# Kernel tuning notes

Hardware: AMD Instinct MI355X
Metric: run time of the kernel (lower is better)

## Reference

```python
import jax, jax.numpy as jnp
import numpy as np

D_MODEL = 1024
N_HEADS = 16
HEAD_DIM = D_MODEL // N_HEADS
D_FF = 4 * D_MODEL
LN_EPS = 1e-5


def setup_inputs() -> dict:
    key = jax.random.key(0)
    ks = jax.random.split(key, 12)
    B, T = 16, 512
    s = lambda fan_in: 1.0 / np.sqrt(fan_in)
    inp = {
        'x': jax.random.normal(ks[0], (B, T, D_MODEL), jnp.float32),
        # torch Linear layout: [out_features, in_features]
        'w_qkv': jax.random.normal(ks[1], (3 * D_MODEL, D_MODEL), jnp.float32) * s(D_MODEL),
        'w_proj': jax.random.normal(ks[2], (D_MODEL, D_MODEL), jnp.float32) * s(D_MODEL),
        'w_ff1': jax.random.normal(ks[3], (D_FF, D_MODEL), jnp.float32) * s(D_MODEL),
        'b_ff1': jax.random.normal(ks[4], (D_FF,), jnp.float32) * 0.02,
        'w_ff2': jax.random.normal(ks[5], (D_MODEL, D_FF), jnp.float32) * s(D_FF),
        'b_ff2': jax.random.normal(ks[6], (D_MODEL,), jnp.float32) * 0.02,
        'ln1_g': jnp.ones((D_MODEL,), jnp.float32),
        'ln1_b': jnp.zeros((D_MODEL,), jnp.float32),
        'ln2_g': jnp.ones((D_MODEL,), jnp.float32),
        'ln2_b': jnp.zeros((D_MODEL,), jnp.float32),
    }
    return inp


def _layernorm(x, g, b):
    mu = jnp.mean(x, axis=-1, keepdims=True)
    var = jnp.var(x, axis=-1, keepdims=True)
    return (x - mu) * jax.lax.rsqrt(var + LN_EPS) * g + b


def _block(x, w_qkv, w_proj, w_ff1, b_ff1, w_ff2, b_ff2, ln1_g, ln1_b, ln2_g, ln2_b):
    B, T, _ = x.shape
    a = _layernorm(x, ln1_g, ln1_b)
    qkv = a @ w_qkv.T  # [B,T,3D]
    q, k, v = jnp.split(qkv, 3, axis=-1)
    # [B,H,T,hd]
    rs = lambda t: t.reshape(B, T, N_HEADS, HEAD_DIM).transpose(0, 2, 1, 3)
    q, k, v = rs(q), rs(k), rs(v)
    scale = HEAD_DIM ** -0.5
    att = jnp.einsum('bhqd,bhkd->bhqk', q, k) * scale
    causal = jnp.tril(jnp.ones((T, T), bool))
    att = jnp.where(causal, att, jnp.float32(-10000.0))
    att = jax.nn.softmax(att, axis=-1)
    out = jnp.einsum('bhqk,bhkd->bhqd', att, v)
    out = out.transpose(0, 2, 1, 3).reshape(B, T, D_MODEL)
    x = x + out @ w_proj.T
    f = _layernorm(x, ln2_g, ln2_b)
    f = jax.nn.gelu(f @ w_ff1.T + b_ff1, approximate=False) @ w_ff2.T + b_ff2
    return x + f


def reference(x, w_qkv, w_proj, w_ff1, b_ff1, w_ff2, b_ff2, ln1_g, ln1_b, ln2_g, ln2_b):
    return _block(x, w_qkv, w_proj, w_ff1, b_ff1, w_ff2, b_ff2, ln1_g, ln1_b, ln2_g, ln2_b)
```

## Files before the change

### kernel.cpp

```cpp
#include <hip/hip_runtime.h>
#include <stdint.h>

typedef __bf16 bf16x8_t __attribute__((ext_vector_type(8)));
typedef float f32x4_t __attribute__((ext_vector_type(4)));
typedef unsigned short ushort8_t __attribute__((ext_vector_type(8)));

#define DEV __device__ __forceinline__

DEV unsigned short f2bf(float f) {
  union { float f; uint32_t u; } v; v.f = f;
  uint32_t r = v.u + 0x7FFFu + ((v.u >> 16) & 1u);
  return (unsigned short)(r >> 16);
}

DEV void gl_lds16(const void* g, void* l) {
  __builtin_amdgcn_global_load_lds(
      (const __attribute__((address_space(1))) void*)g,
      (__attribute__((address_space(3))) void*)l, 16, 0, 0);
}

DEV float gelu_f(float x) {
  const float y = x * 0.7071067811865475f;
  const float ay = fabsf(y);
  const float t = __builtin_amdgcn_rcpf(1.0f + 0.3275911f * ay);
  float p = fmaf(t, 1.061405429f, -1.453152027f);
  p = fmaf(t, p, 1.421413741f);
  p = fmaf(t, p, -0.284496736f);
  p = fmaf(t, p, 0.254829592f);
  p *= t;
  const float e = __expf(-ay * ay);
  float erfv = 1.0f - p * e;
  erfv = copysignf(erfv, y);
  return 0.5f * x * (1.0f + erfv);
}

__global__ __launch_bounds__(256) void cvt_all(const float* __restrict__ w0, unsigned short* __restrict__ o0,
                                               const float* __restrict__ w1, unsigned short* __restrict__ o1,
                                               const float* __restrict__ w2, unsigned short* __restrict__ o2,
                                               const float* __restrict__ w3, unsigned short* __restrict__ o3) {
  int i = blockIdx.x * 256 + threadIdx.x;
  const float* in; unsigned short* outp;
  if (i < 786432) { in = w0; outp = o0; }
  else if (i < 1048576) { in = w1; outp = o1; i -= 786432; }
  else if (i < 2097152) { in = w2; outp = o2; i -= 1048576; }
  else { in = w3; outp = o3; i -= 2097152; }
  float4 v = ((const float4*)in)[i];
  ushort4 o;
  o.x = f2bf(v.x); o.y = f2bf(v.y); o.z = f2bf(v.z); o.w = f2bf(v.w);
  ((ushort4*)outp)[i] = o;
}

__global__ __launch_bounds__(256) void ln_kernel(const float* __restrict__ x,
                                                 const float* __restrict__ g,
                                                 const float* __restrict__ b,
                                                 unsigned short* __restrict__ outp) {
  const int row = blockIdx.x * 4 + (threadIdx.x >> 6);
  const int lane = threadIdx.x & 63;
  const float4* xr = (const float4*)(x + (size_t)row * 1024);
  float4 v[4];
  float s = 0.f, s2 = 0.f;
#pragma unroll
  for (int j = 0; j < 4; ++j) {
    v[j] = xr[j * 64 + lane];
    s += v[j].x + v[j].y + v[j].z + v[j].w;
    s2 += v[j].x * v[j].x + v[j].y * v[j].y + v[j].z * v[j].z + v[j].w * v[j].w;
  }
#pragma unroll
  for (int off = 1; off < 64; off <<= 1) {
    s += __shfl_xor(s, off, 64);
    s2 += __shfl_xor(s2, off, 64);
  }
  const float mu = s * (1.0f / 1024.0f);
  const float var = s2 * (1.0f / 1024.0f) - mu * mu;
  const float rstd = rsqrtf(var + 1e-5f);
  ushort4* orow = (ushort4*)(outp + (size_t)row * 1024);
  const float4* gp = (const float4*)g;
  const float4* bp = (const float4*)b;
#pragma unroll
  for (int j = 0; j < 4; ++j) {
    float4 gv = gp[j * 64 + lane], bv = bp[j * 64 + lane];
    ushort4 o;
    o.x = f2bf((v[j].x - mu) * rstd * gv.x + bv.x);
    o.y = f2bf((v[j].y - mu) * rstd * gv.y + bv.y);
    o.z = f2bf((v[j].z - mu) * rstd * gv.z + bv.z);
    o.w = f2bf((v[j].w - mu) * rstd * gv.w + bv.w);
    orow[j * 64 + lane] = o;
  }
}

template <int MODE>
__global__ __launch_bounds__(256) void gemm_bt(const unsigned short* __restrict__ A,
                                               const unsigned short* __restrict__ B,
                                               float* __restrict__ Cf,
                                               unsigned short* __restrict__ Cb,
                                               const float* __restrict__ bias,
                                               const float* __restrict__ res,
                                               int M, int N, int K) {
  __shared__ unsigned short sA[128 * 32];
  __shared__ unsigned short sB[128 * 32];
  const int tid = threadIdx.x;
  const int w = tid >> 6, lane = tid & 63;
  const int kg = lane >> 4, l16 = lane & 15;
  const int wm = (w & 1) * 64, wn = (w >> 1) * 64;
  const int rowBase = blockIdx.y * 128, colBase = blockIdx.x * 128;

  const int ar = tid >> 2;
  const int ac = (((tid & 3) ^ ((tid >> 3) & 3))) * 8;
  const unsigned short* gA = A + (size_t)(rowBase + ar) * K + ac;
  const unsigned short* gB = B + (size_t)(colBase + ar) * K + ac;
  unsigned short* lA = sA + tid * 8;
  unsigned short* lB = sB + tid * 8;

  f32x4_t acc[4][4];
#pragma unroll
  for (int mi = 0; mi < 4; ++mi)
#pragma unroll
    for (int ni = 0; ni < 4; ++ni) acc[mi][ni] = (f32x4_t)0.0f;

  const unsigned short* pA[4];
  const unsigned short* pB[4];
#pragma unroll
  for (int i = 0; i < 4; ++i) {
    const int rr = wm + i * 16 + l16;
    pA[i] = sA + (rr * 4 + (kg ^ ((l16 >> 1) & 3))) * 8;
    const int cr = wn + i * 16 + l16;
    pB[i] = sB + (cr * 4 + (kg ^ ((l16 >> 1) & 3))) * 8;
  }

  const int nk = K >> 5;
  for (int kt = 0; kt < nk; ++kt) {
    __syncthreads();
    gl_lds16(gA, lA);
    gl_lds16(gA + (size_t)64 * K, lA + 64 * 32);
    gl_lds16(gB, lB);
    gl_lds16(gB + (size_t)64 * K, lB + 64 * 32);
    gA += 32; gB += 32;
    __syncthreads();
    bf16x8_t a[4], b[4];
#pragma unroll
    for (int i = 0; i < 4; ++i) a[i] = *(const bf16x8_t*)pA[i];
#pragma unroll
    for (int i = 0; i < 4; ++i) b[i] = *(const bf16x8_t*)pB[i];
#pragma unroll
    for (int mi = 0; mi < 4; ++mi)
#pragma unroll
      for (int ni = 0; ni < 4; ++ni)
        acc[mi][ni] = __builtin_amdgcn_mfma_f32_16x16x32_bf16(a[mi], b[ni], acc[mi][ni], 0, 0, 0);
  }

#pragma unroll
  for (int mi = 0; mi < 4; ++mi) {
#pragma unroll
    for (int ni = 0; ni < 4; ++ni) {
      const int col = colBase + wn + ni * 16 + l16;
      float bv = 0.f;
      if (MODE == 2 || MODE == 3) bv = bias[col];
#pragma unroll
      for (int r = 0; r < 4; ++r) {
        const int row = rowBase + wm + mi * 16 + kg * 4 + r;
        const size_t idx = (size_t)row * N + col;
        float v = acc[mi][ni][r];
        if (MODE == 0) {
          Cb[idx] = f2bf(v);
        } else if (MODE == 1) {
          Cf[idx] = v + res[idx];
        } else if (MODE == 2) {
          Cb[idx] = f2bf(gelu_f(v + bv));
        } else {
          Cf[idx] = v + bv + res[idx];
        }
      }
    }
  }
}

__global__ __launch_bounds__(256) void attn_kernel(const unsigned short* __restrict__ qkv,
                                                   unsigned short* __restrict__ outp) {
  constexpr int D3 = 3072;
  __shared__ unsigned short sQ[128 * 64];
  __shared__ unsigned short sK[64 * 64];
  __shared__ unsigned short sVt[64 * 72];
  __shared__ unsigned short sP[128 * 72];
  const int tid = threadIdx.x;
  const int w = tid >> 6, lane = tid & 63;
  const int kg = lane >> 4, l16 = lane & 15;
  const int qi = blockIdx.x, h = blockIdx.y, bb = blockIdx.z;
  const int t0 = qi * 128;
  const size_t base = (size_t)bb * 512 * D3 + h * 64;

  const int sr = tid >> 3;
  const int sc = ((tid & 7) ^ ((tid >> 3) & 7)) * 8;

  {
    const unsigned short* g = qkv + base + (size_t)(t0 + sr) * D3 + sc;
    unsigned short* l = sQ + tid * 8;
#pragma unroll
    for (int i = 0; i < 4; ++i) gl_lds16(g + (size_t)32 * i * D3, l + 2048 * i);
  }

  const int wm = w * 32;
  f32x4_t o[2][4];
  float m_i[2][4], l_i[2][4];
#pragma unroll
  for (int mi = 0; mi < 2; ++mi)
#pragma unroll
    for (int r = 0; r < 4; ++r) { m_i[mi][r] = -1e30f; l_i[mi][r] = 0.f; }
#pragma unroll
  for (int mi = 0; mi < 2; ++mi)
#pragma unroll
    for (int di = 0; di < 4; ++di) o[mi][di] = (f32x4_t)0.0f;

  const int nkt = (qi + 1) * 2;
  for (int kt = 0; kt < nkt; ++kt) {
    const int k0 = kt * 64;
    __syncthreads();
    {
      const unsigned short* g = qkv + base + 1024 + (size_t)(k0 + sr) * D3 + sc;
      unsigned short* l = sK + tid * 8;
      gl_lds16(g, l);
      gl_lds16(g + (size_t)32 * D3, l + 2048);
    }
    {
      const int r = tid >> 3, d0 = (tid & 7) * 8;
#pragma unroll
      for (int i = 0; i < 2; ++i) {
        const int k = r + 32 * i;
        ushort8_t v = *(const ushort8_t*)(qkv + base + 2048 + (size_t)(k0 + k) * D3 + d0);
#pragma unroll
        for (int j = 0; j < 8; ++j) sVt[(d0 + j) * 72 + k] = v[j];
      }
    }
    __syncthreads();

    const bool active = (k0 <= t0 + wm + 31);
    if (active) {
      f32x4_t s[2][4];
#pragma unroll
      for (int mi = 0; mi < 2; ++mi)
#pragma unroll
        for (int ni = 0; ni < 4; ++ni) s[mi][ni] = (f32x4_t)0.0f;
#pragma unroll
      for (int kd = 0; kd < 2; ++kd) {
        bf16x8_t aq[2], bk[4];
#pragma unroll
        for (int mi = 0; mi < 2; ++mi) {
          const int rr = wm + mi * 16 + l16;
          aq[mi] = *(const bf16x8_t*)(sQ + (rr * 8 + ((kd * 4 + kg) ^ (l16 & 7))) * 8);
        }
#pragma unroll
        for (int ni = 0; ni < 4; ++ni) {
          const int rr = ni * 16 + l16;
          bk[ni] = *(const bf16x8_t*)(sK + (rr * 8 + ((kd * 4 + kg) ^ (l16 & 7))) * 8);
        }
#pragma unroll
        for (int mi = 0; mi < 2; ++mi)
#pragma unroll
          for (int ni = 0; ni < 4; ++ni)
            s[mi][ni] = __builtin_amdgcn_mfma_f32_16x16x32_bf16(aq[mi], bk[ni], s[mi][ni], 0, 0, 0);
      }
#pragma unroll
      for (int mi = 0; mi < 2; ++mi) {
#pragma unroll
        for (int r = 0; r < 4; ++r) {
          const int q = t0 + wm + mi * 16 + kg * 4 + r;
          float mx = -1e30f;
#pragma unroll
          for (int ni = 0; ni < 4; ++ni) {
            const int kk = k0 + ni * 16 + l16;
            float v = s[mi][ni][r] * 0.125f;
            v = (kk <= q) ? v : -10000.0f;
            s[mi][ni][r] = v;
            mx = fmaxf(mx, v);
          }
#pragma unroll
          for (int off = 1; off < 16; off <<= 1) mx = fmaxf(mx, __shfl_xor(mx, off, 64));
          const float mo = m_i[mi][r];
          const float mn = fmaxf(mo, mx);
          const float alpha = __expf(mo - mn);
          float ps = 0.f;
#pragma unroll
          for (int ni = 0; ni < 4; ++ni) {
            float p = __expf(s[mi][ni][r] - mn);
            s[mi][ni][r] = p;
            ps += p;
          }
#pragma unroll
          for (int off = 1; off < 16; off <<= 1) ps += __shfl_xor(ps, off, 64);
          l_i[mi][r] = l_i[mi][r] * alpha + ps;
          m_i[mi][r] = mn;
#pragma unroll
          for (int di = 0; di < 4; ++di) o[mi][di][r] *= alpha;
          const int prow = wm + mi * 16 + kg * 4 + r;
#pragma unroll
          for (int ni = 0; ni < 4; ++ni)
            sP[prow * 72 + ni * 16 + l16] = f2bf(s[mi][ni][r]);
        }
      }
#pragma unroll
      for (int kd = 0; kd < 2; ++kd) {
        bf16x8_t ap[2], bv[4];
#pragma unroll
        for (int mi = 0; mi < 2; ++mi)
          ap[mi] = *(const bf16x8_t*)(sP + (wm + mi * 16 + l16) * 72 + kd * 32 + kg * 8);
#pragma unroll
        for (int di = 0; di < 4; ++di)
          bv[di] = *(const bf16x8_t*)(sVt + (di * 16 + l16) * 72 + kd * 32 + kg * 8);
#pragma unroll
        for (int mi = 0; mi < 2; ++mi)
#pragma unroll
          for (int di = 0; di < 4; ++di)
            o[mi][di] = __builtin_amdgcn_mfma_f32_16x16x32_bf16(ap[mi], bv[di], o[mi][di], 0, 0, 0);
      }
    }
  }

#pragma unroll
  for (int mi = 0; mi < 2; ++mi) {
#pragma unroll
    for (int r = 0; r < 4; ++r) {
      const float inv = 1.0f / l_i[mi][r];
      const int row = t0 + wm + mi * 16 + kg * 4 + r;
      const size_t ob = ((size_t)bb * 512 + row) * 1024 + h * 64;
#pragma unroll
      for (int di = 0; di < 4; ++di)
        outp[ob + di * 16 + l16] = f2bf(o[mi][di][r] * inv);
    }
  }
}

extern "C" void kernel_launch(void* const* d_in, const int* in_sizes, int n_in,
                              void* d_out, int out_size, void* d_ws, size_t ws_size,
                              hipStream_t stream) {
  const float* x      = (const float*)d_in[0];
  const float* w_qkv  = (const float*)d_in[1];
  const float* w_proj = (const float*)d_in[2];
  const float* w_ff1  = (const float*)d_in[3];
  const float* b_ff1  = (const float*)d_in[4];
  const float* w_ff2  = (const float*)d_in[5];
  const float* b_ff2  = (const float*)d_in[6];
  const float* ln1_g  = (const float*)d_in[7];
  const float* ln1_b  = (const float*)d_in[8];
  const float* ln2_g  = (const float*)d_in[9];
  const float* ln2_b  = (const float*)d_in[10];
  float* out = (float*)d_out;
  char* ws = (char*)d_ws;

  unsigned short* wqkv_b = (unsigned short*)(ws + 0);
  unsigned short* wproj_b = (unsigned short*)(ws + 6291456);
  unsigned short* wff1_b = (unsigned short*)(ws + 8388608);
  unsigned short* wff2_b = (unsigned short*)(ws + 16777216);
  unsigned short* a_b    = (unsigned short*)(ws + 25165824);
  float*          x2_f   = (float*)(ws + 41943040);
  unsigned short* qkv_b  = (unsigned short*)(ws + 75497472);
  unsigned short* attn_b = (unsigned short*)(ws + 125829120);
  unsigned short* h_b    = qkv_b;

  cvt_all<<<12288, 256, 0, stream>>>(w_qkv, wqkv_b, w_proj, wproj_b, w_ff1, wff1_b, w_ff2, wff2_b);

  ln_kernel<<<2048, 256, 0, stream>>>(x, ln1_g, ln1_b, a_b);
  gemm_bt<0><<<dim3(24, 64), 256, 0, stream>>>(a_b, wqkv_b, nullptr, qkv_b, nullptr, nullptr, 8192, 3072, 1024);
  attn_kernel<<<dim3(4, 16, 16), 256, 0, stream>>>(qkv_b, attn_b);
  gemm_bt<1><<<dim3(8, 64), 256, 0, stream>>>(attn_b, wproj_b, x2_f, nullptr, nullptr, x, 8192, 1024, 1024);
  ln_kernel<<<2048, 256, 0, stream>>>(x2_f, ln2_g, ln2_b, a_b);
  gemm_bt<2><<<dim3(32, 64), 256, 0, stream>>>(a_b, wff1_b, nullptr, h_b, b_ff1, nullptr, 8192, 4096, 1024);
  gemm_bt<3><<<dim3(8, 64), 256, 0, stream>>>(h_b, wff2_b, out, nullptr, b_ff2, x2_f, 8192, 1024, 4096);
}
```

Baseline: 523.5 us.

## Emit transposed V from QKV GEMM epilogue and double GEMM K-tile to 64

The QKV GEMM epilogue now writes the V third of the output directly in a per-head transposed layout into a scratch buffer that aliases x2_f, which is not yet written at that point. The attention kernel can then load V^T into LDS with async global-to-LDS copies instead of scalar transposing stores. Separately, the GEMM K tile grows from 32 to 64 with an 8-chunk XOR swizzle, halving the number of barrier-separated k iterations at the cost of doubled LDS per block. Both changes are meant to cut LDS-store and synchronization overhead.

```diff
diff --git a/kernel.cpp b/kernel.cpp
--- a/kernel.cpp
+++ b/kernel.cpp
@@ -95,19 +95,20 @@
                                                unsigned short* __restrict__ Cb,
                                                const float* __restrict__ bias,
                                                const float* __restrict__ res,
+                                               unsigned short* __restrict__ Vt,
                                                int M, int N, int K) {
-  __shared__ unsigned short sA[128 * 32];
-  __shared__ unsigned short sB[128 * 32];
+  __shared__ unsigned short sA[128 * 64];
+  __shared__ unsigned short sB[128 * 64];
   const int tid = threadIdx.x;
   const int w = tid >> 6, lane = tid & 63;
   const int kg = lane >> 4, l16 = lane & 15;
   const int wm = (w & 1) * 64, wn = (w >> 1) * 64;
   const int rowBase = blockIdx.y * 128, colBase = blockIdx.x * 128;
 
-  const int ar = tid >> 2;
-  const int ac = (((tid & 3) ^ ((tid >> 3) & 3))) * 8;
-  const unsigned short* gA = A + (size_t)(rowBase + ar) * K + ac;
-  const unsigned short* gB = B + (size_t)(colBase + ar) * K + ac;
+  const int sr = tid >> 3;
+  const int scc = ((tid & 7) ^ (sr & 7)) * 8;
+  const unsigned short* gA = A + (size_t)(rowBase + sr) * K + scc;
+  const unsigned short* gB = B + (size_t)(colBase + sr) * K + scc;
   unsigned short* lA = sA + tid * 8;
   unsigned short* lB = sB + tid * 8;
 
@@ -117,35 +118,40 @@
 #pragma unroll
     for (int ni = 0; ni < 4; ++ni) acc[mi][ni] = (f32x4_t)0.0f;
 
-  const unsigned short* pA[4];
-  const unsigned short* pB[4];
-#pragma unroll
-  for (int i = 0; i < 4; ++i) {
-    const int rr = wm + i * 16 + l16;
-    pA[i] = sA + (rr * 4 + (kg ^ ((l16 >> 1) & 3))) * 8;
-    const int cr = wn + i * 16 + l16;
-    pB[i] = sB + (cr * 4 + (kg ^ ((l16 >> 1) & 3))) * 8;
-  }
-
-  const int nk = K >> 5;
+  const unsigned short* pA[2][4];
+  const unsigned short* pB[2][4];
+#pragma unroll
+  for (int kd = 0; kd < 2; ++kd)
+#pragma unroll
+    for (int i = 0; i < 4; ++i) {
+      const int kc = kd * 4 + kg;
+      pA[kd][i] = sA + (wm + i * 16 + l16) * 64 + ((kc ^ (l16 & 7)) * 8);
+      pB[kd][i] = sB + (wn + i * 16 + l16) * 64 + ((kc ^ (l16 & 7)) * 8);
+    }
+
+  const int nk = K >> 6;
   for (int kt = 0; kt < nk; ++kt) {
     __syncthreads();
-    gl_lds16(gA, lA);
-    gl_lds16(gA + (size_t)64 * K, lA + 64 * 32);
-    gl_lds16(gB, lB);
-    gl_lds16(gB + (size_t)64 * K, lB + 64 * 32);
-    gA += 32; gB += 32;
+#pragma unroll
+    for (int i = 0; i < 4; ++i) {
+      gl_lds16(gA + (size_t)(32 * i) * K, lA + 2048 * i);
+      gl_lds16(gB + (size_t)(32 * i) * K, lB + 2048 * i);
+    }
+    gA += 64; gB += 64;
     __syncthreads();
-    bf16x8_t a[4], b[4];
-#pragma unroll
-    for (int i = 0; i < 4; ++i) a[i] = *(const bf16x8_t*)pA[i];
-#pragma unroll
-    for (int i = 0; i < 4; ++i) b[i] = *(const bf16x8_t*)pB[i];
-#pragma unroll
-    for (int mi = 0; mi < 4; ++mi)
-#pragma unroll
-      for (int ni = 0; ni < 4; ++ni)
-        acc[mi][ni] = __builtin_amdgcn_mfma_f32_16x16x32_bf16(a[mi], b[ni], acc[mi][ni], 0, 0, 0);
+#pragma unroll
+    for (int kd = 0; kd < 2; ++kd) {
+      bf16x8_t a[4], b[4];
+#pragma unroll
+      for (int i = 0; i < 4; ++i) a[i] = *(const bf16x8_t*)pA[kd][i];
+#pragma unroll
+      for (int i = 0; i < 4; ++i) b[i] = *(const bf16x8_t*)pB[kd][i];
+#pragma unroll
+      for (int mi = 0; mi < 4; ++mi)
+#pragma unroll
+        for (int ni = 0; ni < 4; ++ni)
+          acc[mi][ni] = __builtin_amdgcn_mfma_f32_16x16x32_bf16(a[mi], b[ni], acc[mi][ni], 0, 0, 0);
+    }
   }
 
 #pragma unroll
@@ -153,6 +159,18 @@
 #pragma unroll
     for (int ni = 0; ni < 4; ++ni) {
       const int col = colBase + wn + ni * 16 + l16;
+      if (MODE == 0 && colBase >= 2048) {
+        const int c2 = col - 2048;
+        const int hh = c2 >> 6, dd = c2 & 63;
+        const int rw = rowBase + wm + mi * 16 + kg * 4;
+        ushort4 pk;
+        pk.x = f2bf(acc[mi][ni][0]);
+        pk.y = f2bf(acc[mi][ni][1]);
+        pk.z = f2bf(acc[mi][ni][2]);
+        pk.w = f2bf(acc[mi][ni][3]);
+        *(ushort4*)(Vt + (((size_t)(rw >> 9) * 16 + hh) * 64 + dd) * 512 + (rw & 511)) = pk;
+        continue;
+      }
       float bv = 0.f;
       if (MODE == 2 || MODE == 3) bv = bias[col];
 #pragma unroll
@@ -175,11 +193,12 @@
 }
 
 __global__ __launch_bounds__(256) void attn_kernel(const unsigned short* __restrict__ qkv,
+                                                   const unsigned short* __restrict__ Vt,
                                                    unsigned short* __restrict__ outp) {
   constexpr int D3 = 3072;
   __shared__ unsigned short sQ[128 * 64];
   __shared__ unsigned short sK[64 * 64];
-  __shared__ unsigned short sVt[64 * 72];
+  __shared__ unsigned short sVt[64 * 64];
   __shared__ unsigned short sP[128 * 72];
   const int tid = threadIdx.x;
   const int w = tid >> 6, lane = tid & 63;
@@ -189,7 +208,7 @@
   const size_t base = (size_t)bb * 512 * D3 + h * 64;
 
   const int sr = tid >> 3;
-  const int sc = ((tid & 7) ^ ((tid >> 3) & 7)) * 8;
+  const int sc = ((tid & 7) ^ (sr & 7)) * 8;
 
   {
     const unsigned short* g = qkv + base + (size_t)(t0 + sr) * D3 + sc;
@@ -197,6 +216,8 @@
 #pragma unroll
     for (int i = 0; i < 4; ++i) gl_lds16(g + (size_t)32 * i * D3, l + 2048 * i);
   }
+
+  const unsigned short* gVbase = Vt + ((size_t)(bb * 16 + h) * 64 + sr) * 512 + sc;
 
   const int wm = w * 32;
   f32x4_t o[2][4];
@@ -221,14 +242,10 @@
       gl_lds16(g + (size_t)32 * D3, l + 2048);
     }
     {
-      const int r = tid >> 3, d0 = (tid & 7) * 8;
-#pragma unroll
-      for (int i = 0; i < 2; ++i) {
-        const int k = r + 32 * i;
-        ushort8_t v = *(const ushort8_t*)(qkv + base + 2048 + (size_t)(k0 + k) * D3 + d0);
-#pragma unroll
-        for (int j = 0; j < 8; ++j) sVt[(d0 + j) * 72 + k] = v[j];
-      }
+      const unsigned short* g = gVbase + k0;
+      unsigned short* l = sVt + tid * 8;
+      gl_lds16(g, l);
+      gl_lds16(g + (size_t)32 * 512, l + 2048);
     }
     __syncthreads();
 
@@ -245,12 +262,12 @@
 #pragma unroll
         for (int mi = 0; mi < 2; ++mi) {
           const int rr = wm + mi * 16 + l16;
-          aq[mi] = *(const bf16x8_t*)(sQ + (rr * 8 + ((kd * 4 + kg) ^ (l16 & 7))) * 8);
+          aq[mi] = *(const bf16x8_t*)(sQ + rr * 64 + (((kd * 4 + kg) ^ (l16 & 7)) * 8));
         }
 #pragma unroll
         for (int ni = 0; ni < 4; ++ni) {
           const int rr = ni * 16 + l16;
-          bk[ni] = *(const bf16x8_t*)(sK + (rr * 8 + ((kd * 4 + kg) ^ (l16 & 7))) * 8);
+          bk[ni] = *(const bf16x8_t*)(sK + rr * 64 + (((kd * 4 + kg) ^ (l16 & 7)) * 8));
         }
 #pragma unroll
         for (int mi = 0; mi < 2; ++mi)
@@ -303,8 +320,10 @@
         for (int mi = 0; mi < 2; ++mi)
           ap[mi] = *(const bf16x8_t*)(sP + (wm + mi * 16 + l16) * 72 + kd * 32 + kg * 8);
 #pragma unroll
-        for (int di = 0; di < 4; ++di)
-          bv[di] = *(const bf16x8_t*)(sVt + (di * 16 + l16) * 72 + kd * 32 + kg * 8);
+        for (int di = 0; di < 4; ++di) {
+          const int dd = di * 16 + l16;
+          bv[di] = *(const bf16x8_t*)(sVt + dd * 64 + (((kd * 4 + kg) ^ (l16 & 7)) * 8));
+        }
 #pragma unroll
         for (int mi = 0; mi < 2; ++mi)
 #pragma unroll
@@ -345,23 +364,24 @@
   float* out = (float*)d_out;
   char* ws = (char*)d_ws;
 
-  unsigned short* wqkv_b = (unsigned short*)(ws + 0);
+  unsigned short* wqkv_b  = (unsigned short*)(ws + 0);
   unsigned short* wproj_b = (unsigned short*)(ws + 6291456);
-  unsigned short* wff1_b = (unsigned short*)(ws + 8388608);
-  unsigned short* wff2_b = (unsigned short*)(ws + 16777216);
-  unsigned short* a_b    = (unsigned short*)(ws + 25165824);
-  float*          x2_f   = (float*)(ws + 41943040);
-  unsigned short* qkv_b  = (unsigned short*)(ws + 75497472);
-  unsigned short* attn_b = (unsigned short*)(ws + 125829120);
-  unsigned short* h_b    = qkv_b;
+  unsigned short* wff1_b  = (unsigned short*)(ws + 8388608);
+  unsigned short* wff2_b  = (unsigned short*)(ws + 16777216);
+  unsigned short* a_b     = (unsigned short*)(ws + 25165824);
+  float*          x2_f    = (float*)(ws + 41943040);
+  unsigned short* vt_b    = (unsigned short*)(ws + 41943040);
+  unsigned short* qkv_b   = (unsigned short*)(ws + 75497472);
+  unsigned short* attn_b  = (unsigned short*)(ws + 125829120);
+  unsigned short* h_b     = qkv_b;
 
   cvt_all<<<12288, 256, 0, stream>>>(w_qkv, wqkv_b, w_proj, wproj_b, w_ff1, wff1_b, w_ff2, wff2_b);
 
   ln_kernel<<<2048, 256, 0, stream>>>(x, ln1_g, ln1_b, a_b);
-  gemm_bt<0><<<dim3(24, 64), 256, 0, stream>>>(a_b, wqkv_b, nullptr, qkv_b, nullptr, nullptr, 8192, 3072, 1024);
-  attn_kernel<<<dim3(4, 16, 16), 256, 0, stream>>>(qkv_b, attn_b);
-  gemm_bt<1><<<dim3(8, 64), 256, 0, stream>>>(attn_b, wproj_b, x2_f, nullptr, nullptr, x, 8192, 1024, 1024);
+  gemm_bt<0><<<dim3(24, 64), 256, 0, stream>>>(a_b, wqkv_b, nullptr, qkv_b, nullptr, nullptr, vt_b, 8192, 3072, 1024);
+  attn_kernel<<<dim3(4, 16, 16), 256, 0, stream>>>(qkv_b, vt_b, attn_b);
+  gemm_bt<1><<<dim3(8, 64), 256, 0, stream>>>(attn_b, wproj_b, x2_f, nullptr, nullptr, x, nullptr, 8192, 1024, 1024);
   ln_kernel<<<2048, 256, 0, stream>>>(x2_f, ln2_g, ln2_b, a_b);
-  gemm_bt<2><<<dim3(32, 64), 256, 0, stream>>>(a_b, wff1_b, nullptr, h_b, b_ff1, nullptr, 8192, 4096, 1024);
-  gemm_bt<3><<<dim3(8, 64), 256, 0, stream>>>(h_b, wff2_b, out, nullptr, b_ff2, x2_f, 8192, 1024, 4096);
-}
+  gemm_bt<2><<<dim3(32, 64), 256, 0, stream>>>(a_b, wff1_b, nullptr, h_b, b_ff1, nullptr, nullptr, 8192, 4096, 1024);
+  gemm_bt<3><<<dim3(8, 64), 256, 0, stream>>>(h_b, wff2_b, out, nullptr, b_ff2, x2_f, nullptr, 8192, 1024, 4096);
+}
```

After: 497.0 us. 5.1% less time.
